# Optimization experiments

Measured on AMD Instinct MI355X. Metric: run time of the kernel, lower is better.

The kernel has to match this reference:

```python
import jax, jax.numpy as jnp
import numpy as np

B, T, C, NH = 8, 1024, 768, 12
HD = C // NH
NEG = -1e9


def setup_inputs() -> dict:
    key = jax.random.key(0)
    ks = jax.random.split(key, 8)
    s_c = 1.0 / np.sqrt(C)
    s_t = 1.0 / np.sqrt(T)
    return {
        "x": jax.random.normal(ks[0], (B, T, C), dtype=jnp.float32),
        "Wv": jax.random.normal(ks[1], (C, C), dtype=jnp.float32) * s_c,
        "bv": jnp.zeros((C,), dtype=jnp.float32),
        "Wl": jax.random.normal(ks[2], (T, T), dtype=jnp.float32) * s_t,  # weights_layer, no bias
        "Wc": jax.random.normal(ks[3], (T, T), dtype=jnp.float32) * s_t,  # weight_concat
        "bc": jnp.zeros((T,), dtype=jnp.float32),
        "Wp": jax.random.normal(ks[4], (C, C), dtype=jnp.float32) * s_c,
        "bp": jnp.zeros((C,), dtype=jnp.float32),
    }


def reference(x, Wv, bv, Wl, Wc, bc, Wp, bp):
    Bq, Tq, Cq = x.shape
    # NOTE: original forward uses self.value(x) for q, k, and v alike.
    v = x @ Wv.T + bv                              # [B,T,C]
    q = k = v
    # split heads -> [B, nh, T, hd]
    def heads(t):
        return t.reshape(Bq, Tq, NH, HD).transpose(0, 2, 1, 3)
    qh, kh, vh = heads(q), heads(k), heads(v)
    att = jnp.einsum("bhqd,bhkd->bhqk", qh, kh) / jnp.sqrt(jnp.float32(HD))
    # learned seqlen-mixing over the key dim: Linear(T,T) acts on last axis
    att = att @ Wl.T                               # weights_layer (no bias)
    att = att @ Wc.T + bc                          # weight_concat
    # causal mask (tril)
    causal = jnp.tril(jnp.ones((Tq, Tq), dtype=bool))
    att = jnp.where(causal[None, None], att, NEG)
    att = jax.nn.softmax(att, axis=-1)             # attn_drop is identity at eval
    y = jnp.einsum("bhqk,bhkd->bhqd", att, vh)
    y = y.transpose(0, 2, 1, 3).reshape(Bq, Tq, Cq)
    return y @ Wp.T + bp                           # resid_drop identity at eval
```

## Files before the change

### kernel.cpp

```cpp
#include <hip/hip_runtime.h>
#include <stdint.h>

#define Bz 8
#define Tz 1024
#define Cz 768
#define NHz 12
#define HDz 64

typedef unsigned short u16;
typedef __attribute__((ext_vector_type(8))) __bf16 bf16x8;
typedef __attribute__((ext_vector_type(4))) float f32x4;
typedef __attribute__((ext_vector_type(4))) unsigned int u32x4;

__device__ __forceinline__ float bf2f(u16 b) {
    union { uint32_t u; float f; } c; c.u = ((uint32_t)b) << 16; return c.f;
}
__device__ __forceinline__ u16 f2bf(float f) {
    union { float f; uint32_t u; } c; c.f = f;
    uint32_t u = c.u;
    return (u16)((u + 0x7fffu + ((u >> 16) & 1u)) >> 16);
}
__device__ __forceinline__ u16 f2bf_hw(float f) {
    __bf16 b = (__bf16)f;
    union { __bf16 b; u16 u; } c; c.b = b; return c.u;
}

#define N4_X  (Bz * Tz * Cz / 4)
#define N4_WV (Cz * Cz / 4)
#define N4_WC (Tz * Tz / 4)
#define N4_WP (Cz * Cz / 4)
#define N4_ALL (N4_X + N4_WV + N4_WC + N4_WP)

__global__ __launch_bounds__(256)
void cvt_all(const float* __restrict__ x, const float* __restrict__ wv,
             const float* __restrict__ wc, const float* __restrict__ wp,
             u16* __restrict__ xb, u16* __restrict__ wvb,
             u16* __restrict__ wcb, u16* __restrict__ wpb) {
    int i = blockIdx.x * 256 + threadIdx.x;
    if (i >= N4_ALL) return;
    const float* in;
    u16* out;
    if (i < N4_X) {
        in = x; out = xb;
    } else if (i < N4_X + N4_WV) {
        in = wv; out = wvb; i -= N4_X;
    } else if (i < N4_X + N4_WV + N4_WC) {
        in = wc; out = wcb; i -= N4_X + N4_WV;
    } else {
        in = wp; out = wpb; i -= N4_X + N4_WV + N4_WC;
    }
    float4 v = ((const float4*)in)[i];
    union { u16 h[4]; uint2 u; } o;
    o.h[0] = f2bf(v.x); o.h[1] = f2bf(v.y); o.h[2] = f2bf(v.z); o.h[3] = f2bf(v.w);
    ((uint2*)out)[i] = o.u;
}

template<int BM, int BN, int WM, int WN, bool OUTF32, bool HASBIAS>
__global__ __launch_bounds__(WM * WN * 64)
void gemm_bt(const u16* __restrict__ A, long long sAz, int lda,
             const u16* __restrict__ Bp, long long sBz, int ldb,
             void* __restrict__ Cp, long long sCz, int ldc,
             const float* __restrict__ bias, int K, float alpha) {
    constexpr int NT = WM * WN * 64;
    constexpr int BK = 64;
    constexpr int AI = (BM * BK) / (NT * 8);
    constexpr int BI = (BN * BK) / (NT * 8);
    static_assert(AI >= 1 && (BM * BK) % (NT * 8) == 0, "A staging");
    static_assert(BI >= 1 && (BN * BK) % (NT * 8) == 0, "B staging");
    static_assert(BM == WM * 64 && BN == WN * 64, "wave tiling");

    __shared__ alignas(16) u16 As[2][BM * BK];
    __shared__ alignas(16) u16 Bs[2][BN * BK];

    const int z = blockIdx.z;
    const u16* Ag = A + (long long)z * sAz;
    const u16* Bg = Bp + (long long)z * sBz;

    const int tid = threadIdx.x;
    const int lane = tid & 63;
    const int w = tid >> 6;
    const int wm = w / WN;
    const int wn = w % WN;
    const int rowBase = blockIdx.y * BM;
    const int colBase = blockIdx.x * BN;
    const int quad = lane >> 4;
    const int frow = lane & 15;

    auto stage = [&](int buf, int k0) {
#pragma unroll
        for (int i = 0; i < AI; i++) {
            int e = (i * NT + tid) * 8;
            int row = e >> 6;
            int gcol = (((e & 63) >> 3) ^ (row & 7)) * 8;
            const u16* g = Ag + (long long)(rowBase + row) * lda + k0 + gcol;
            __builtin_amdgcn_global_load_lds(
                (const __attribute__((address_space(1))) uint32_t*)g,
                (__attribute__((address_space(3))) uint32_t*)(&As[buf][0] + e), 16, 0, 0);
        }
#pragma unroll
        for (int i = 0; i < BI; i++) {
            int e = (i * NT + tid) * 8;
            int row = e >> 6;
            int gcol = (((e & 63) >> 3) ^ (row & 7)) * 8;
            const u16* g = Bg + (long long)(colBase + row) * ldb + k0 + gcol;
            __builtin_amdgcn_global_load_lds(
                (const __attribute__((address_space(1))) uint32_t*)g,
                (__attribute__((address_space(3))) uint32_t*)(&Bs[buf][0] + e), 16, 0, 0);
        }
    };

    f32x4 acc[4][4] = {};

    const int nk = K / BK;
    stage(0, 0);
    __syncthreads();

#pragma unroll 1
    for (int t = 0; t < nk; ++t) {
        const int cur = t & 1;
        if (t + 1 < nk) stage(cur ^ 1, (t + 1) * BK);

#pragma unroll
        for (int kk = 0; kk < 2; kk++) {
            bf16x8 af[4], bfr[4];
#pragma unroll
            for (int mt = 0; mt < 4; mt++) {
                int row = wm * 64 + mt * 16 + frow;
                af[mt] = *(const bf16x8*)&As[cur][row * 64 + (((kk * 4 + quad) ^ (frow & 7)) * 8)];
            }
#pragma unroll
            for (int nt = 0; nt < 4; nt++) {
                int row = wn * 64 + nt * 16 + frow;
                bfr[nt] = *(const bf16x8*)&Bs[cur][row * 64 + (((kk * 4 + quad) ^ (frow & 7)) * 8)];
            }
#pragma unroll
            for (int mt = 0; mt < 4; mt++)
#pragma unroll
                for (int nt = 0; nt < 4; nt++)
                    acc[mt][nt] = __builtin_amdgcn_mfma_f32_16x16x32_bf16(
                        af[mt], bfr[nt], acc[mt][nt], 0, 0, 0);
        }

        __syncthreads();
    }

    const int r0 = rowBase + wm * 64;
    const int c0 = colBase + wn * 64;
    const int rl = (lane >> 4) * 4;
    const int cl = lane & 15;
#pragma unroll
    for (int mt = 0; mt < 4; mt++) {
#pragma unroll
        for (int nt = 0; nt < 4; nt++) {
#pragma unroll
            for (int r = 0; r < 4; r++) {
                int row = r0 + mt * 16 + rl + r;
                int col = c0 + nt * 16 + cl;
                float v = acc[mt][nt][r] * alpha;
                if (HASBIAS) v += bias[col];
                if (OUTF32)
                    ((float*)Cp)[(long long)z * sCz + (long long)row * ldc + col] = v;
                else
                    ((u16*)Cp)[(long long)z * sCz + (long long)row * ldc + col] = f2bf_hw(v);
            }
        }
    }
}

template<bool INF32>
__global__ __launch_bounds__(256)
void transpose_to_bf16(const void* __restrict__ in, u16* __restrict__ out,
                       int rows, int cols, long long sInZ, long long sOutZ) {
    __shared__ u16 tile[32][33];
    const int z = blockIdx.z;
    const int c0 = blockIdx.x * 32, r0 = blockIdx.y * 32;
    const int tx = threadIdx.x, ty = threadIdx.y;
#pragma unroll
    for (int i = 0; i < 32; i += 8) {
        long long off = (long long)z * sInZ + (long long)(r0 + ty + i) * cols + c0 + tx;
        tile[ty + i][tx] = INF32 ? f2bf(((const float*)in)[off]) : ((const u16*)in)[off];
    }
    __syncthreads();
#pragma unroll
    for (int i = 0; i < 32; i += 8)
        out[(long long)z * sOutZ + (long long)(c0 + ty + i) * rows + r0 + tx] = tile[tx][ty + i];
}

#define LOG2E 1.44269504f

__global__ __launch_bounds__(512)
void flash_attn(const u16* __restrict__ v, const u16* __restrict__ U,
                const u16* __restrict__ vT, const float* __restrict__ bc,
                u16* __restrict__ y) {
    __shared__ alignas(16) u16 Us[128 * 64];
    __shared__ alignas(16) u16 Vs[64 * 128];
    __shared__ alignas(16) u16 Ps[128 * 136];
    __shared__ u16 bcs[Tz];

    const int bi = blockIdx.x;
    const int xcd = bi & 7;
    const int slot = bi >> 3;
    const int col = (slot % 12) * 8 + xcd;
    const int qi = 7 - slot / 12;
    const int b = col / NHz, h = col % NHz;

    const int tid = threadIdx.x, lane = tid & 63, w = tid >> 6;
    const int quad = lane >> 4, cl = lane & 15;
    const int q0 = qi * 128;
    const int wrow = w * 16;

    for (int j = tid; j < Tz; j += 512) bcs[j] = f2bf(bc[j] * LOG2E);

    const u16* vq = v + ((long long)b * Tz + q0) * Cz + h * HDz;
    bf16x8 aS[2];
#pragma unroll
    for (int ks = 0; ks < 2; ks++)
        aS[ks] = *(const bf16x8*)(vq + (long long)(wrow + cl) * Cz + ks * 32 + quad * 8);

    f32x4 Oacc[4] = {};
    float mrow[4], lrow[4];
#pragma unroll
    for (int r = 0; r < 4; r++) { mrow[r] = -3.0e38f; lrow[r] = 0.f; }

    const u16* Ub = U + (long long)b * Tz * Cz + h * HDz;
    const u16* Vb = vT + ((long long)b * Cz + h * HDz) * Tz;

    __syncthreads();

    const int kts = qi + 1;
    for (int kt = 0; kt < kts; kt++) {
        if (kt) __builtin_amdgcn_s_barrier();
        const u16* Ug = Ub + (long long)kt * 128 * Cz;
#pragma unroll
        for (int i = 0; i < 2; i++) {
            int e = (i * 512 + tid) * 8;
            int key = e >> 6;
            int ch = ((e & 63) >> 3) ^ (key & 7);
            __builtin_amdgcn_global_load_lds(
                (const __attribute__((address_space(1))) uint32_t*)(Ug + (long long)key * Cz + ch * 8),
                (__attribute__((address_space(3))) uint32_t*)(Us + e), 16, 0, 0);
        }
        const u16* Vg = Vb + kt * 128;
#pragma unroll
        for (int i = 0; i < 2; i++) {
            int e = (i * 512 + tid) * 8;
            int dim = e >> 7;
            int ch = ((e & 127) >> 3) ^ (dim & 15);
            __builtin_amdgcn_global_load_lds(
                (const __attribute__((address_space(1))) uint32_t*)(Vg + (long long)dim * Tz + ch * 8),
                (__attribute__((address_space(3))) uint32_t*)(Vs + e), 16, 0, 0);
        }
        asm volatile("s_waitcnt vmcnt(2)" ::: "memory");
        __builtin_amdgcn_s_barrier();

        f32x4 S[8] = {};
        __builtin_amdgcn_s_setprio(1);
#pragma unroll
        for (int ks = 0; ks < 2; ks++)
#pragma unroll
            for (int nt = 0; nt < 8; nt++) {
                int key = nt * 16 + cl;
                bf16x8 bS = *(const bf16x8*)&Us[key * 64 + (((ks * 4 + quad) ^ (key & 7)) * 8)];
                S[nt] = __builtin_amdgcn_mfma_f32_16x16x32_bf16(aS[ks], bS, S[nt], 0, 0, 0);
            }
        __builtin_amdgcn_s_setprio(0);

        const bool last = (kt == kts - 1);
#pragma unroll
        for (int nt = 0; nt < 8; nt++) {
            float bl = bf2f(bcs[kt * 128 + nt * 16 + cl]);
#pragma unroll
            for (int r = 0; r < 4; r++)
                S[nt][r] = S[nt][r] * (0.125f * LOG2E) + bl;
        }
        if (last) {
            int rowg = q0 + wrow + quad * 4;
#pragma unroll
            for (int nt = 0; nt < 8; nt++) {
                int colg = kt * 128 + nt * 16 + cl;
#pragma unroll
                for (int r = 0; r < 4; r++)
                    if (colg > rowg + r) S[nt][r] = -3.0e38f;
            }
        }

        float mnew[4], alpha[4];
#pragma unroll
        for (int r = 0; r < 4; r++) {
            float m = S[0][r];
#pragma unroll
            for (int nt = 1; nt < 8; nt++) m = fmaxf(m, S[nt][r]);
#pragma unroll
            for (int d = 1; d < 16; d <<= 1) m = fmaxf(m, __shfl_xor(m, d));
            mnew[r] = fmaxf(mrow[r], m);
            alpha[r] = __builtin_amdgcn_exp2f(mrow[r] - mnew[r]);
            mrow[r] = mnew[r];
        }

        float psum[4] = {};
#pragma unroll
        for (int nt = 0; nt < 8; nt++)
#pragma unroll
            for (int r = 0; r < 4; r++) {
                float p = __builtin_amdgcn_exp2f(S[nt][r] - mnew[r]);
                psum[r] += p;
                Ps[(wrow + quad * 4 + r) * 136 + nt * 16 + cl] = f2bf_hw(p);
            }
#pragma unroll
        for (int r = 0; r < 4; r++) {
            float s = psum[r];
#pragma unroll
            for (int d = 1; d < 16; d <<= 1) s += __shfl_xor(s, d);
            lrow[r] = lrow[r] * alpha[r] + s;
#pragma unroll
            for (int nt2 = 0; nt2 < 4; nt2++)
                Oacc[nt2][r] *= alpha[r];
        }

        asm volatile("s_waitcnt vmcnt(0)" ::: "memory");
        __builtin_amdgcn_s_barrier();

        __builtin_amdgcn_s_setprio(1);
#pragma unroll
        for (int ks = 0; ks < 4; ks++) {
            bf16x8 pA = *(const bf16x8*)&Ps[(wrow + cl) * 136 + ks * 32 + quad * 8];
#pragma unroll
            for (int nt2 = 0; nt2 < 4; nt2++) {
                int dim = nt2 * 16 + cl;
                bf16x8 vB = *(const bf16x8*)&Vs[dim * 128 + (((ks * 4 + quad) ^ cl) * 8)];
                Oacc[nt2] = __builtin_amdgcn_mfma_f32_16x16x32_bf16(pA, vB, Oacc[nt2], 0, 0, 0);
            }
        }
        __builtin_amdgcn_s_setprio(0);
    }

    u16* yq = y + ((long long)b * Tz + q0) * Cz + h * HDz;
#pragma unroll
    for (int r = 0; r < 4; r++) {
        float inv = 1.f / lrow[r];
#pragma unroll
        for (int nt2 = 0; nt2 < 4; nt2++)
            yq[(long long)(wrow + quad * 4 + r) * Cz + nt2 * 16 + cl] =
                f2bf_hw(Oacc[nt2][r] * inv);
    }
}

extern "C" void kernel_launch(void* const* d_in, const int* in_sizes, int n_in,
                              void* d_out, int out_size, void* d_ws, size_t ws_size,
                              hipStream_t stream) {
    const float* x  = (const float*)d_in[0];
    const float* Wv = (const float*)d_in[1];
    const float* bv = (const float*)d_in[2];
    const float* Wl = (const float*)d_in[3];
    const float* Wc = (const float*)d_in[4];
    const float* bc = (const float*)d_in[5];
    const float* Wp = (const float*)d_in[6];
    const float* bp = (const float*)d_in[7];

    u16* ws  = (u16*)d_ws;
    u16* xb  = ws;
    u16* Wvb = xb  + (size_t)Bz * Tz * Cz;
    u16* Wcb = Wvb + (size_t)Cz * Cz;
    u16* Wpb = Wcb + (size_t)Tz * Tz;
    u16* WlT = Wpb + (size_t)Cz * Cz;
    u16* Wcl = WlT + (size_t)Tz * Tz;
    u16* vbf = Wcl + (size_t)Tz * Tz;
    u16* vT  = vbf + (size_t)Bz * Tz * Cz;
    u16* U   = vT  + (size_t)Bz * Tz * Cz;

    const long long sTC = (long long)Tz * Cz;
    const long long sCT = (long long)Cz * Tz;

    cvt_all<<<(N4_ALL + 255) / 256, 256, 0, stream>>>(x, Wv, Wc, Wp, xb, Wvb, Wcb, Wpb);
    transpose_to_bf16<true><<<dim3(32, 32, 1), dim3(32, 8), 0, stream>>>(Wl, WlT, Tz, Tz, 0, 0);
    gemm_bt<64, 64, 1, 1, false, false><<<dim3(Tz / 64, Tz / 64, 1), 64, 0, stream>>>(
        Wcb, 0, Tz, WlT, 0, Tz, Wcl, 0, Tz, nullptr, Tz, 1.f);
    gemm_bt<128, 128, 2, 2, false, true><<<dim3(Cz / 128, (Bz * Tz) / 128, 1), 256, 0, stream>>>(
        xb, 0, Cz, Wvb, 0, Cz, vbf, 0, Cz, bv, Cz, 1.f);
    transpose_to_bf16<false><<<dim3(Cz / 32, Tz / 32, Bz), dim3(32, 8), 0, stream>>>(
        vbf, vT, Tz, Cz, sTC, sCT);
    gemm_bt<128, 128, 2, 2, false, false><<<dim3(Cz / 128, Tz / 128, Bz), 256, 0, stream>>>(
        Wcl, 0, Tz, vT, sCT, Tz, U, sTC, Cz, nullptr, Tz, 1.f);
    flash_attn<<<dim3(8 * NHz * Bz, 1, 1), 512, 0, stream>>>(vbf, U, vT, bc, vbf);
    gemm_bt<128, 128, 2, 2, true, true><<<dim3(Cz / 128, (Bz * Tz) / 128, 1), 256, 0, stream>>>(
        vbf, 0, Cz, Wpb, 0, Cz, (float*)d_out, 0, Cz, bp, Cz, 1.f);
}
```

Measured before the change: 221.3 us.

## Prefetch two K-tiles ahead in GEMM with fine-grained vmcnt waits

Restructures the bf16 GEMM main loop so each iteration first loads all LDS fragments for both k-substeps into registers, then barriers, and only then issues the async global->LDS load for tile t+2 into the buffer just read. Explicit s_waitcnt on vmcnt replaces full __syncthreads, so the loads for the next tile can stay in flight across iterations. The aim is to hide global load latency behind MFMA work. The cost is double the fragment registers per wave and hand-encoded waitcnt fields that must match the gfx950 counter layout.

```diff
diff --git a/kernel.cpp b/kernel.cpp
--- a/kernel.cpp
+++ b/kernel.cpp
@@ -23,6 +23,14 @@
 __device__ __forceinline__ u16 f2bf_hw(float f) {
     __bf16 b = (__bf16)f;
     union { __bf16 b; u16 u; } c; c.b = b; return c.u;
+}
+
+template<unsigned VM>
+__device__ __forceinline__ void wait_vm() {
+    __builtin_amdgcn_s_waitcnt((VM & 15u) | (7u << 4) | (15u << 8) | ((VM >> 4) << 14));
+}
+__device__ __forceinline__ void wait_lgkm0() {
+    __builtin_amdgcn_s_waitcnt(15u | (7u << 4) | (0u << 8) | (3u << 14));
 }
 
 #define N4_X  (Bz * Tz * Cz / 4)
@@ -65,6 +73,7 @@
     constexpr int BK = 64;
     constexpr int AI = (BM * BK) / (NT * 8);
     constexpr int BI = (BN * BK) / (NT * 8);
+    constexpr unsigned LD = AI + BI;
     static_assert(AI >= 1 && (BM * BK) % (NT * 8) == 0, "A staging");
     static_assert(BI >= 1 && (BN * BK) % (NT * 8) == 0, "B staging");
     static_assert(BM == WM * 64 && BN == WN * 64, "wave tiling");
@@ -113,35 +122,45 @@
 
     const int nk = K / BK;
     stage(0, 0);
-    __syncthreads();
+    if (nk > 1) { stage(1, BK); wait_vm<LD>(); }
+    else        { wait_vm<0>(); }
+    __builtin_amdgcn_s_barrier();
 
 #pragma unroll 1
     for (int t = 0; t < nk; ++t) {
         const int cur = t & 1;
-        if (t + 1 < nk) stage(cur ^ 1, (t + 1) * BK);
-
+
+        bf16x8 af[2][4], bfr[2][4];
 #pragma unroll
         for (int kk = 0; kk < 2; kk++) {
-            bf16x8 af[4], bfr[4];
 #pragma unroll
             for (int mt = 0; mt < 4; mt++) {
                 int row = wm * 64 + mt * 16 + frow;
-                af[mt] = *(const bf16x8*)&As[cur][row * 64 + (((kk * 4 + quad) ^ (frow & 7)) * 8)];
+                af[kk][mt] = *(const bf16x8*)&As[cur][row * 64 + (((kk * 4 + quad) ^ (frow & 7)) * 8)];
             }
 #pragma unroll
             for (int nt = 0; nt < 4; nt++) {
                 int row = wn * 64 + nt * 16 + frow;
-                bfr[nt] = *(const bf16x8*)&Bs[cur][row * 64 + (((kk * 4 + quad) ^ (frow & 7)) * 8)];
-            }
+                bfr[kk][nt] = *(const bf16x8*)&Bs[cur][row * 64 + (((kk * 4 + quad) ^ (frow & 7)) * 8)];
+            }
+        }
+        wait_lgkm0();
+        __builtin_amdgcn_s_barrier();
+
+        if (t + 2 < nk) stage(cur, (t + 2) * BK);
+
+#pragma unroll
+        for (int kk = 0; kk < 2; kk++)
 #pragma unroll
             for (int mt = 0; mt < 4; mt++)
 #pragma unroll
                 for (int nt = 0; nt < 4; nt++)
                     acc[mt][nt] = __builtin_amdgcn_mfma_f32_16x16x32_bf16(
-                        af[mt], bfr[nt], acc[mt][nt], 0, 0, 0);
-        }
-
-        __syncthreads();
+                        af[kk][mt], bfr[kk][nt], acc[mt][nt], 0, 0, 0);
+
+        if (t + 2 < nk)       wait_vm<LD>();
+        else if (t + 1 < nk)  wait_vm<0>();
+        if (t + 1 < nk) __builtin_amdgcn_s_barrier();
     }
 
     const int r0 = rowBase + wm * 64;
```

New measurement: 210.6 us. -4.8%, faster.
